# Performance work log

Hardware: AMD Instinct MI355X
Metric: run time of the kernel (lower is better)

The kernel has to match this reference:

```python
import jax, jax.numpy as jnp
import numpy as np

# MAML backbone parameter shapes (standard 4-conv few-shot net + 5-way logits head)
PARAM_SHAPES = [(64, 3, 3, 3), (64,), (64, 64, 3, 3), (64,), (64, 64, 3, 3), (64,),
                (64, 64, 3, 3), (64,), (5, 1600), (5,)]
GATE_DIM = 512   # hierarchicalClustering.input_dim + hidden_dim
B = 256          # meta-batch of tasks (vectorized over the original python loop)


def setup_inputs() -> dict:
    key = jax.random.key(0)
    ks = jax.random.split(key, 1 + 3 * len(PARAM_SHAPES))
    inp = {"emb": jax.random.normal(ks[0], (B, GATE_DIM), dtype=jnp.float32)}
    for i, s in enumerate(PARAM_SHAPES):
        n = int(np.prod(s))
        inp[f"p{i}"] = jax.random.normal(ks[1 + 3 * i], s, dtype=jnp.float32) * 0.05
        inp[f"W{i}"] = jax.random.normal(ks[2 + 3 * i], (n, GATE_DIM), dtype=jnp.float32) / np.float32(np.sqrt(GATE_DIM))
        inp[f"b{i}"] = jnp.zeros((n,), dtype=jnp.float32)
    return inp


def reference(emb, p0, W0, b0, p1, W1, b1, p2, W2, b2, p3, W3, b3, p4, W4, b4,
              p5, W5, b5, p6, W6, b6, p7, W7, b7, p8, W8, b8, p9, W9, b9):
    # Per MAML parameter tensor: eta = sigmoid(Linear(emb)); adapted = eta * theta.
    # Loop is over a small fixed set of structurally distinct params (10), vectorized over tasks B.
    triples = [(p0, W0, b0), (p1, W1, b1), (p2, W2, b2), (p3, W3, b3), (p4, W4, b4),
               (p5, W5, b5), (p6, W6, b6), (p7, W7, b7), (p8, W8, b8), (p9, W9, b9)]
    outs = []
    for p, W, b in triples:
        eta = jax.nn.sigmoid(emb @ W.T + b)          # [B, numel_i]
        outs.append(eta * p.reshape(-1))             # adapted theta_i, flattened
    return jnp.concatenate(outs, axis=1)             # [B, total_numel]
```

## Files before the change

### kernel.cpp

```cpp
#include <hip/hip_runtime.h>
#include <hip/hip_bf16.h>

#define GATE 512
#define MROWS 256
#define NTOT 120581

typedef __attribute__((ext_vector_type(8))) short short8;
typedef __attribute__((ext_vector_type(4))) float  f32x4;

struct GemmParams {
    const float* W[10];
    const float* p[10];
    const float* bias[10];
};

__device__ __forceinline__ short bf16bits(float x) {
    __hip_bfloat16 h = __float2bfloat16(x);
    return *reinterpret_cast<short*>(&h);
}

__global__ void emb_to_bf16(const float* __restrict__ emb,
                            unsigned short* __restrict__ o) {
    int i = (blockIdx.x * blockDim.x + threadIdx.x) * 8;
    f32x4 a = *(const f32x4*)(emb + i);
    f32x4 b = *(const f32x4*)(emb + i + 4);
    short8 r;
#pragma unroll
    for (int j = 0; j < 4; ++j) { r[j] = bf16bits(a[j]); r[4 + j] = bf16bits(b[j]); }
    *(short8*)(o + i) = r;
}

__global__ __launch_bounds__(256, 4) void gate_gemm(GemmParams P,
                                                    const unsigned short* __restrict__ embw,
                                                    float* __restrict__ out)
{
    constexpr int kStarts[11] = {0, 1728, 1792, 38656, 38720, 75584,
                                 75648, 112512, 112576, 120576, 120581};
    __shared__ unsigned short Atile[2][MROWS * 32];

    const int t    = threadIdx.x;
    const int lane = t & 63;
    const int wave = t >> 6;
    const int lr   = lane & 15;
    const int lg   = lane >> 4;

    const int  n     = blockIdx.x * 64 + wave * 16 + lr;
    const bool valid = n < NTOT;
    const int  nc    = valid ? n : NTOT - 1;
    int tt = 0;
#pragma unroll
    for (int i = 1; i < 10; ++i) tt += (nc >= kStarts[i]);
    const int rr = nc - kStarts[tt];
    const float* wrow = P.W[tt] + (size_t)rr * GATE + lg * 8;
    const float pv = P.p[tt][rr];
    const float bv = P.bias[tt][rr];

    const int srow  = t >> 2;
    const int sslot = (t & 3) ^ ((t >> 3) & 3);
    const unsigned short* asrc = embw + (size_t)srow * GATE + sslot * 8;

    const int aslot = lg ^ ((lr >> 1) & 3);
    const int abase = lr * 32 + aslot * 8;

    f32x4 acc[16];
#pragma unroll
    for (int i = 0; i < 16; ++i) acc[i] = (f32x4){0.f, 0.f, 0.f, 0.f};

    auto stage = [&](int buf, int kb) {
#pragma unroll
        for (int i = 0; i < 4; ++i) {
            const unsigned short* src = asrc + (size_t)i * 64 * GATE + kb;
            unsigned short* dst = &Atile[buf][(size_t)(i * 256 + t) * 8];
            __builtin_amdgcn_global_load_lds(
                (const __attribute__((address_space(1))) void*)src,
                (__attribute__((address_space(3))) void*)dst, 16, 0, 0);
        }
    };

    stage(0, 0);
    f32x4 b0 = *(const f32x4*)(wrow);
    f32x4 b1 = *(const f32x4*)(wrow + 4);
    __syncthreads();

    int buf = 0;
#pragma unroll
    for (int ks = 0; ks < 16; ++ks) {
        f32x4 nb0, nb1;
        if (ks < 15) {
            stage(buf ^ 1, (ks + 1) * 32);
            nb0 = *(const f32x4*)(wrow + (ks + 1) * 32);
            nb1 = *(const f32x4*)(wrow + (ks + 1) * 32 + 4);
        }

        short8 bfrag;
#pragma unroll
        for (int j = 0; j < 4; ++j) {
            bfrag[j]     = bf16bits(b0[j]);
            bfrag[4 + j] = bf16bits(b1[j]);
        }

        const unsigned short* ab = &Atile[buf][abase];
#pragma unroll
        for (int mf = 0; mf < 16; ++mf) {
            short8 afrag = *(const short8*)(ab + mf * 512);
            acc[mf] = __builtin_amdgcn_mfma_f32_16x16x32_bf16(afrag, bfrag, acc[mf], 0, 0, 0);
        }

        __syncthreads();
        b0 = nb0; b1 = nb1;
        buf ^= 1;
    }

    if (valid) {
        float* ocol = out + n;
#pragma unroll
        for (int mf = 0; mf < 16; ++mf) {
            const int m0 = mf * 16 + lg * 4;
#pragma unroll
            for (int q = 0; q < 4; ++q) {
                float x   = acc[mf][q] + bv;
                float e   = __expf(-x);
                float eta = __builtin_amdgcn_rcpf(1.0f + e);
                ocol[(size_t)(m0 + q) * NTOT] = eta * pv;
            }
        }
    }
}

extern "C" void kernel_launch(void* const* d_in, const int* in_sizes, int n_in,
                              void* d_out, int out_size, void* d_ws, size_t ws_size,
                              hipStream_t stream) {
    const float* emb = (const float*)d_in[0];
    GemmParams P;
    for (int i = 0; i < 10; ++i) {
        P.p[i]    = (const float*)d_in[1 + 3 * i];
        P.W[i]    = (const float*)d_in[2 + 3 * i];
        P.bias[i] = (const float*)d_in[3 + 3 * i];
    }

    unsigned short* embw = (unsigned short*)d_ws;
    emb_to_bf16<<<(MROWS * GATE) / (256 * 8), 256, 0, stream>>>(emb, embw);

    int nblocks = (NTOT + 63) / 64;
    gate_gemm<<<nblocks, 256, 0, stream>>>(P, embw, (float*)d_out);
}
```

Measured before the change: 131.3 us.

## Keep full-K bf16 weight fragments in registers and stream emb rows in chunks

Restructures the gate GEMM so each lane converts its entire 512-long weight row to bf16 once and holds it in 16 registers. The emb matrix is streamed through LDS in 16-row chunks covering the full K, with a new XOR swizzle. Each chunk yields one finished 16x16 accumulator tile, so sigmoid and stores happen per chunk, interleaved with the MFMA work. The aim is to drop the 16-register accumulator array, overlap output writes with compute, and convert each weight only once. The trade-off is more LDS traffic per MFMA, a barrier per chunk, and removal of the occupancy hint from launch bounds.

```diff
diff --git a/kernel.cpp b/kernel.cpp
--- a/kernel.cpp
+++ b/kernel.cpp
@@ -4,6 +4,8 @@
 #define GATE 512
 #define MROWS 256
 #define NTOT 120581
+#define CH 16
+#define NCH 16
 
 typedef __attribute__((ext_vector_type(8))) short short8;
 typedef __attribute__((ext_vector_type(4))) float  f32x4;
@@ -30,13 +32,13 @@
     *(short8*)(o + i) = r;
 }
 
-__global__ __launch_bounds__(256, 4) void gate_gemm(GemmParams P,
-                                                    const unsigned short* __restrict__ embw,
-                                                    float* __restrict__ out)
+__global__ __launch_bounds__(256) void gate_gemm(GemmParams P,
+                                                 const unsigned short* __restrict__ embw,
+                                                 float* __restrict__ out)
 {
     constexpr int kStarts[11] = {0, 1728, 1792, 38656, 38720, 75584,
                                  75648, 112512, 112576, 120576, 120581};
-    __shared__ unsigned short Atile[2][MROWS * 32];
+    __shared__ unsigned short Atile[2][CH * GATE];
 
     const int t    = threadIdx.x;
     const int lane = t & 63;
@@ -55,21 +57,12 @@
     const float pv = P.p[tt][rr];
     const float bv = P.bias[tt][rr];
 
-    const int srow  = t >> 2;
-    const int sslot = (t & 3) ^ ((t >> 3) & 3);
-    const unsigned short* asrc = embw + (size_t)srow * GATE + sslot * 8;
-
-    const int aslot = lg ^ ((lr >> 1) & 3);
-    const int abase = lr * 32 + aslot * 8;
-
-    f32x4 acc[16];
-#pragma unroll
-    for (int i = 0; i < 16; ++i) acc[i] = (f32x4){0.f, 0.f, 0.f, 0.f};
-
-    auto stage = [&](int buf, int kb) {
+    auto stage = [&](int buf, int c) {
 #pragma unroll
         for (int i = 0; i < 4; ++i) {
-            const unsigned short* src = asrc + (size_t)i * 64 * GATE + kb;
+            const int rl = i * 4 + wave;
+            const unsigned short* src =
+                embw + (size_t)(c * CH + rl) * GATE + ((lane ^ (rl & 7)) * 8);
             unsigned short* dst = &Atile[buf][(size_t)(i * 256 + t) * 8];
             __builtin_amdgcn_global_load_lds(
                 (const __attribute__((address_space(1))) void*)src,
@@ -78,52 +71,57 @@
     };
 
     stage(0, 0);
-    f32x4 b0 = *(const f32x4*)(wrow);
-    f32x4 b1 = *(const f32x4*)(wrow + 4);
+
+    short8 Bbf[16];
+#pragma unroll
+    for (int b = 0; b < 4; ++b) {
+        f32x4 raw[8];
+#pragma unroll
+        for (int j = 0; j < 4; ++j) {
+            raw[j * 2 + 0] = *(const f32x4*)(wrow + (b * 4 + j) * 32);
+            raw[j * 2 + 1] = *(const f32x4*)(wrow + (b * 4 + j) * 32 + 4);
+        }
+#pragma unroll
+        for (int j = 0; j < 4; ++j) {
+            short8 bb;
+#pragma unroll
+            for (int q = 0; q < 4; ++q) {
+                bb[q]     = bf16bits(raw[j * 2][q]);
+                bb[4 + q] = bf16bits(raw[j * 2 + 1][q]);
+            }
+            Bbf[b * 4 + j] = bb;
+        }
+    }
+
     __syncthreads();
 
     int buf = 0;
 #pragma unroll
-    for (int ks = 0; ks < 16; ++ks) {
-        f32x4 nb0, nb1;
-        if (ks < 15) {
-            stage(buf ^ 1, (ks + 1) * 32);
-            nb0 = *(const f32x4*)(wrow + (ks + 1) * 32);
-            nb1 = *(const f32x4*)(wrow + (ks + 1) * 32 + 4);
-        }
+    for (int c = 0; c < NCH; ++c) {
+        if (c + 1 < NCH) stage(buf ^ 1, c + 1);
 
-        short8 bfrag;
+        f32x4 acc = (f32x4){0.f, 0.f, 0.f, 0.f};
 #pragma unroll
-        for (int j = 0; j < 4; ++j) {
-            bfrag[j]     = bf16bits(b0[j]);
-            bfrag[4 + j] = bf16bits(b1[j]);
-        }
-
-        const unsigned short* ab = &Atile[buf][abase];
-#pragma unroll
-        for (int mf = 0; mf < 16; ++mf) {
-            short8 afrag = *(const short8*)(ab + mf * 512);
-            acc[mf] = __builtin_amdgcn_mfma_f32_16x16x32_bf16(afrag, bfrag, acc[mf], 0, 0, 0);
+        for (int ks = 0; ks < 16; ++ks) {
+            const int slot = (ks * 4 + lg) ^ (lr & 7);
+            short8 af = *(const short8*)(&Atile[buf][lr * GATE + slot * 8]);
+            acc = __builtin_amdgcn_mfma_f32_16x16x32_bf16(af, Bbf[ks], acc, 0, 0, 0);
         }
 
         __syncthreads();
-        b0 = nb0; b1 = nb1;
-        buf ^= 1;
-    }
 
-    if (valid) {
-        float* ocol = out + n;
-#pragma unroll
-        for (int mf = 0; mf < 16; ++mf) {
-            const int m0 = mf * 16 + lg * 4;
+        if (valid) {
+            float* ocol = out + n;
+            const int m0 = c * CH + lg * 4;
 #pragma unroll
             for (int q = 0; q < 4; ++q) {
-                float x   = acc[mf][q] + bv;
+                float x   = acc[q] + bv;
                 float e   = __expf(-x);
                 float eta = __builtin_amdgcn_rcpf(1.0f + e);
                 ocol[(size_t)(m0 + q) * NTOT] = eta * pv;
             }
         }
+        buf ^= 1;
     }
 }
 
```

Result: faster. 119.3 us (-9.2%).
